# Kernel tuning notes

Hardware: AMD Instinct MI355X
Metric: run time of the kernel (lower is better)

Reference implementation:

```python
import jax, jax.numpy as jnp
import numpy as np

K_KP = 4            # sample_keypoints
RADIUS = 2.0        # sample_radius_m
FEATURE_LEVELS = 2
NUM_HEADS = 8


def _keypoints():
    return jnp.array([[0.0, 0.0, 0.0], [RADIUS, 0.0, 0.0],
                      [0.0, RADIUS, 0.0], [-RADIUS, 0.0, 0.0]], jnp.float32)[:K_KP]


def _bilinear(fmap, grid):
    # fmap [C,H,W], grid [N,2] in [-1,1], align_corners=True, zero padding
    C, H, W = fmap.shape
    x = (grid[:, 0] + 1.0) * 0.5 * (W - 1)
    y = (grid[:, 1] + 1.0) * 0.5 * (H - 1)
    x0 = jnp.floor(x); y0 = jnp.floor(y)
    wx1 = x - x0; wx0 = 1.0 - wx1
    wy1 = y - y0; wy0 = 1.0 - wy1

    def get(xi, yi):
        inb = (xi >= 0) & (xi <= W - 1) & (yi >= 0) & (yi <= H - 1)
        xc = jnp.clip(xi, 0, W - 1).astype(jnp.int32)
        yc = jnp.clip(yi, 0, H - 1).astype(jnp.int32)
        return fmap[:, yc, xc] * inb.astype(fmap.dtype)  # [C,N]

    out = (get(x0, y0) * (wx0 * wy0) + get(x0 + 1, y0) * (wx1 * wy0)
           + get(x0, y0 + 1) * (wx0 * wy1) + get(x0 + 1, y0 + 1) * (wx1 * wy1))
    return out.T  # [N,C]


def _sample_level(fmap, refs, intrinsics, extrinsics):
    # fmap [B,V,C,H,W], refs [B,N,3] with N = Q*K_KP
    B, V, C, H, W = fmap.shape
    N = refs.shape[1]
    ph = jnp.concatenate([refs, jnp.ones((B, N, 1), refs.dtype)], -1)     # [B,N,4]
    cam = jnp.einsum('bvij,bnj->bvni', extrinsics, ph)[..., :3]            # [B,V,N,3]
    uvw = jnp.einsum('bvij,bvnj->bvni', intrinsics, cam)                   # [B,V,N,3]
    z = uvw[..., 2]
    zs = jnp.where(jnp.abs(z) > 1e-6, z, 1e-6)
    gx = 2.0 * (uvw[..., 0] / zs) / (W - 1) - 1.0
    gy = 2.0 * (uvw[..., 1] / zs) / (H - 1) - 1.0
    grid = jnp.stack([gx, gy], -1)                                         # [B,V,N,2]
    samp = jax.vmap(jax.vmap(_bilinear))(fmap, grid)                       # [B,V,N,C]
    valid = (z > 0.0).astype(fmap.dtype)                                   # [B,V,N]
    Q = N // K_KP
    samp = samp.reshape(B, V, Q, K_KP, C)
    valid = valid.reshape(B, V, Q, K_KP)
    s = jnp.einsum('bvqkc,bvqk->bqc', samp, valid)
    cnt = jnp.maximum(valid.sum(axis=(1, 3)), 1.0)[..., None]              # [B,Q,1]
    return s / cnt


def _sampler(features, refs_xyz, intrinsics, extrinsics):
    B, Q = refs_xyz.shape[:2]
    refs = (refs_xyz[:, :, None, :] + _keypoints()[None, None]).reshape(B, Q * K_KP, 3)
    out = jnp.zeros((B, Q, features[0].shape[2]), refs_xyz.dtype)
    for fmap in features[:FEATURE_LEVELS]:
        out = out + _sample_level(fmap, refs, intrinsics, extrinsics)
    return out / float(FEATURE_LEVELS)


def _cross_attn(q_in, ctx, Wq, bq, Wk, bk, Wv, bv, Wo, bo):
    B, Qn, D = q_in.shape
    Kn = ctx.shape[1]
    hd = D // NUM_HEADS
    q = (q_in @ Wq.T + bq).reshape(B, Qn, NUM_HEADS, hd).transpose(0, 2, 1, 3)
    k = (ctx @ Wk.T + bk).reshape(B, Kn, NUM_HEADS, hd).transpose(0, 2, 1, 3)
    v = (ctx @ Wv.T + bv).reshape(B, Kn, NUM_HEADS, hd).transpose(0, 2, 1, 3)
    scores = jnp.einsum('bhqd,bhkd->bhqk', q, k) / jnp.sqrt(jnp.asarray(hd, q.dtype))
    attn = jax.nn.softmax(scores, axis=-1)
    o = jnp.einsum('bhqk,bhkd->bhqd', attn, v).transpose(0, 2, 1, 3).reshape(B, Qn, D)
    return o @ Wo.T + bo


def setup_inputs() -> dict:
    key = jax.random.key(0)
    ks = jax.random.split(key, 10)
    B, V, C, Q = 2, 6, 256, 900
    features0 = jax.random.normal(ks[0], (B, V, C, 64, 176), jnp.float32)
    features1 = jax.random.normal(ks[1], (B, V, C, 32, 88), jnp.float32)
    refs_xyz = jax.random.uniform(ks[2], (B, Q, 3), jnp.float32, -1.0, 1.0) * jnp.array([50.0, 50.0, 1.5])
    K = np.array([[1000.0, 0.0, 800.0], [0.0, 1000.0, 450.0], [0.0, 0.0, 1.0]], np.float32)
    intrinsics = jnp.asarray(np.broadcast_to(K, (B, V, 3, 3)).copy())
    axes = np.array([[0.0, -1.0, 0.0], [0.0, 0.0, -1.0], [1.0, 0.0, 0.0]], np.float32)
    exts = np.zeros((V, 4, 4), np.float32)
    for vi in range(V):
        yaw = 2.0 * np.pi * vi / V
        Rz = np.array([[np.cos(yaw), np.sin(yaw), 0.0], [-np.sin(yaw), np.cos(yaw), 0.0], [0.0, 0.0, 1.0]], np.float32)
        exts[vi, :3, :3] = axes @ Rz
        exts[vi, 3, 3] = 1.0
    extrinsics = jnp.asarray(np.broadcast_to(exts, (B, V, 4, 4)).copy())
    queries = jax.random.normal(ks[3], (B, Q, C), jnp.float32)
    Wq = jax.random.normal(ks[4], (C, C), jnp.float32) * 0.02
    Wk = jax.random.normal(ks[5], (C, C), jnp.float32) * 0.02
    Wv = jax.random.normal(ks[6], (C, C), jnp.float32) * 0.02
    Wo = jax.random.normal(ks[7], (C, C), jnp.float32) * 0.02
    z = jnp.zeros((C,), jnp.float32)
    return {"features0": features0, "features1": features1, "refs_xyz": refs_xyz,
            "intrinsics": intrinsics, "extrinsics": extrinsics, "queries": queries,
            "Wq": Wq, "bq": z, "Wk": Wk, "bk": z, "Wv": Wv, "bv": z, "Wo": Wo, "bo": z}


def reference(features0, features1, refs_xyz, intrinsics, extrinsics, queries,
              Wq, bq, Wk, bk, Wv, bv, Wo, bo):
    sampled = _sampler([features0, features1], refs_xyz, intrinsics, extrinsics)  # [B,Q,C]
    return _cross_attn(queries, sampled, Wq, bq, Wk, bk, Wv, bv, Wo, bo)
```

## Files before the change

kernel.cpp:

```cpp
#include <hip/hip_runtime.h>
#include <math.h>

#define B 2
#define V 6
#define C 256
#define Q 900
#define NH 8
#define HD 32
#define RADIUS 2.0f
#define M_ROWS (B * Q)
#define NT 29
#define SPLITS 4
#define TPS 8

using short8 = __attribute__((ext_vector_type(8))) short;
using f32x4  = __attribute__((ext_vector_type(4))) float;

__device__ __forceinline__ short f2bf(float f) {
    union { float f; unsigned u; } x; x.f = f;
    unsigned r = x.u + 0x7fffu + ((x.u >> 16) & 1u);
    return (short)(r >> 16);
}

__device__ __forceinline__ float kpx(int k) { return (k == 1) ? RADIUS : ((k == 3) ? -RADIUS : 0.f); }
__device__ __forceinline__ float kpy(int k) { return (k == 2) ? RADIUS : 0.f; }

__device__ __forceinline__ float tapv(const float* __restrict__ base, float xi, float yi, int W, int H) {
    if (xi < 0.f || xi > (float)(W - 1) || yi < 0.f || yi > (float)(H - 1)) return 0.f;
    int xc = (int)xi, yc = (int)yi;
    return base[yc * W + xc];
}

__global__ __launch_bounds__(256)
void sampler_kernel(const float* __restrict__ f0, const float* __restrict__ f1,
                    const float* __restrict__ refs, const float* __restrict__ intr,
                    const float* __restrict__ extr, float* __restrict__ sampled)
{
    int b = blockIdx.x / Q, q = blockIdx.x % Q;
    int t = threadIdx.x;
    __shared__ float sx0[2][24], sy0[2][24], swx1[2][24], swy1[2][24];
    __shared__ float sval[24];

    if (t < 48) {
        int lvl = t / 24, pt = t % 24;
        int v = pt >> 2, kp = pt & 3;
        const float* r = refs + (size_t)(b * Q + q) * 3;
        float px = r[0] + kpx(kp), py = r[1] + kpy(kp), pz = r[2];
        const float* E = extr + (size_t)(b * V + v) * 16;
        float cx = E[0] * px + E[1] * py + E[2]  * pz + E[3];
        float cy = E[4] * px + E[5] * py + E[6]  * pz + E[7];
        float cz = E[8] * px + E[9] * py + E[10] * pz + E[11];
        const float* Km = intr + (size_t)(b * V + v) * 9;
        float u = Km[0] * cx + Km[1] * cy + Km[2] * cz;
        float w = Km[3] * cx + Km[4] * cy + Km[5] * cz;
        float z = Km[6] * cx + Km[7] * cy + Km[8] * cz;
        float zs = (fabsf(z) > 1e-6f) ? z : 1e-6f;
        float ru = u / zs, rv = w / zs;
        const float Wf = lvl ? 87.f : 175.f;
        const float Hf = lvl ? 31.f : 63.f;
        float gx = 2.f * ru / Wf - 1.f;
        float gy = 2.f * rv / Hf - 1.f;
        float x = (gx + 1.f) * 0.5f * Wf;
        float y = (gy + 1.f) * 0.5f * Hf;
        float x0 = floorf(x), y0 = floorf(y);
        sx0[lvl][pt] = x0;  sy0[lvl][pt] = y0;
        swx1[lvl][pt] = x - x0;  swy1[lvl][pt] = y - y0;
        if (lvl == 0) sval[pt] = (z > 0.f) ? 1.f : 0.f;
    }
    __syncthreads();

    float cnt = 0.f;
    #pragma unroll
    for (int i = 0; i < 24; ++i) cnt += sval[i];
    cnt = fmaxf(cnt, 1.f);
    float icnt = 1.f / cnt;

    float acc_total = 0.f;
    #pragma unroll
    for (int lvl = 0; lvl < 2; ++lvl) {
        const int H = lvl ? 32 : 64;
        const int W = lvl ? 88 : 176;
        const int HW = H * W;
        const float* fm = lvl ? f1 : f0;

        float accl = 0.f;
        for (int i = 0; i < 24; ++i) {
            if (sval[i] == 0.f) continue;
            int v = i >> 2;
            float x0 = sx0[lvl][i], y0 = sy0[lvl][i];
            float wx1 = swx1[lvl][i], wy1 = swy1[lvl][i];
            float wx0 = 1.f - wx1, wy0 = 1.f - wy1;
            const float* base = fm + ((size_t)(b * V + v) * C + t) * (size_t)HW;
            accl += tapv(base, x0,       y0,       W, H) * (wx0 * wy0)
                  + tapv(base, x0 + 1.f, y0,       W, H) * (wx1 * wy0)
                  + tapv(base, x0,       y0 + 1.f, W, H) * (wx0 * wy1)
                  + tapv(base, x0 + 1.f, y0 + 1.f, W, H) * (wx1 * wy1);
        }
        acc_total += accl * icnt;
    }
    sampled[(size_t)(b * Q + q) * C + t] = acc_total * 0.5f;
}

__global__ __launch_bounds__(256)
void wpack4(const float* __restrict__ W0, const float* __restrict__ W1,
            const float* __restrict__ W2, const float* __restrict__ W3,
            short* __restrict__ P0, short* __restrict__ P1,
            short* __restrict__ P2, short* __restrict__ P3)
{
    int gid = blockIdx.x * 256 + threadIdx.x;
    int mat = gid >> 13;
    int rem = gid & 8191;
    int ks = rem >> 10;
    int nt = (rem >> 6) & 15;
    int lane = rem & 63;
    const float* W = (mat == 0) ? W0 : (mat == 1) ? W1 : (mat == 2) ? W2 : W3;
    short* P = (mat == 0) ? P0 : (mat == 1) ? P1 : (mat == 2) ? P2 : P3;
    int n = nt * 16 + (lane & 15);
    int k0 = ks * 32 + 8 * (lane >> 4);
    float4 a = *(const float4*)(W + (size_t)n * C + k0);
    float4 b = *(const float4*)(W + (size_t)n * C + k0 + 4);
    short8 s;
    s[0] = f2bf(a.x); s[1] = f2bf(a.y); s[2] = f2bf(a.z); s[3] = f2bf(a.w);
    s[4] = f2bf(b.x); s[5] = f2bf(b.y); s[6] = f2bf(b.z); s[7] = f2bf(b.w);
    *(short8*)(P + (size_t)((ks * 16 + nt) * 64 + lane) * 8) = s;
}

__device__ __forceinline__ void mgemm_body(const float* __restrict__ A,
                                           const short* __restrict__ Wp,
                                           const float* __restrict__ bias,
                                           float* __restrict__ Y,
                                           int m0, int n0t)
{
    __shared__ __align__(16) short As[64][264];
    const int tid = threadIdx.x;
    const int lane = tid & 63, w = tid >> 6;
    const int l15 = lane & 15, g = lane >> 4;

    {
        int r = tid & 63, part = tid >> 6;
        int gm = m0 + r;
        #pragma unroll
        for (int c = 0; c < 8; ++c) {
            int k = part * 64 + c * 8;
            float4 x = make_float4(0.f, 0.f, 0.f, 0.f);
            float4 y = make_float4(0.f, 0.f, 0.f, 0.f);
            if (gm < M_ROWS) {
                x = *(const float4*)(A + (size_t)gm * C + k);
                y = *(const float4*)(A + (size_t)gm * C + k + 4);
            }
            short8 s;
            s[0] = f2bf(x.x); s[1] = f2bf(x.y); s[2] = f2bf(x.z); s[3] = f2bf(x.w);
            s[4] = f2bf(y.x); s[5] = f2bf(y.y); s[6] = f2bf(y.z); s[7] = f2bf(y.w);
            *(short8*)&As[r][k] = s;
        }
    }
    __syncthreads();

    f32x4 acc[4];
    #pragma unroll
    for (int c = 0; c < 4; ++c) acc[c] = (f32x4){0.f, 0.f, 0.f, 0.f};

    #pragma unroll
    for (int ks = 0; ks < 8; ++ks) {
        short8 af = *(const short8*)&As[16 * w + l15][ks * 32 + 8 * g];
        #pragma unroll
        for (int c = 0; c < 4; ++c) {
            int nt = n0t * 4 + c;
            short8 bf = *(const short8*)(Wp + (size_t)((ks * 16 + nt) * 64 + lane) * 8);
            acc[c] = __builtin_amdgcn_mfma_f32_16x16x32_bf16(af, bf, acc[c], 0, 0, 0);
        }
    }

    #pragma unroll
    for (int c = 0; c < 4; ++c) {
        int n = n0t * 64 + c * 16 + l15;
        float bv = bias[n];
        #pragma unroll
        for (int j = 0; j < 4; ++j) {
            int gm = m0 + 16 * w + 4 * g + j;
            if (gm < M_ROWS) Y[(size_t)gm * C + n] = acc[c][j] + bv;
        }
    }
}

__global__ __launch_bounds__(256)
void gemm_qkv_mfma(const float* __restrict__ Xq, const float* __restrict__ Xs,
                   const short* __restrict__ Pq, const short* __restrict__ Pk,
                   const short* __restrict__ Pv,
                   const float* __restrict__ bq, const float* __restrict__ bk,
                   const float* __restrict__ bv,
                   float* __restrict__ Yq, float* __restrict__ Yk, float* __restrict__ Yv)
{
    int z = blockIdx.z;
    const float* A    = (z == 0) ? Xq : Xs;
    const short* Wp   = (z == 0) ? Pq : (z == 1) ? Pk : Pv;
    const float* bias = (z == 0) ? bq : (z == 1) ? bk : bv;
    float* Y          = (z == 0) ? Yq : (z == 1) ? Yk : Yv;
    mgemm_body(A, Wp, bias, Y, blockIdx.x * 64, blockIdx.y);
}

__global__ __launch_bounds__(256)
void gemm_o_mfma(const float* __restrict__ A, const short* __restrict__ Wp,
                 const float* __restrict__ bias, float* __restrict__ Y)
{
    mgemm_body(A, Wp, bias, Y, blockIdx.x * 64, blockIdx.y);
}

__global__ __launch_bounds__(128)
void attn_mfma_split(const float* __restrict__ qb, const float* __restrict__ kb,
                     const float* __restrict__ vb,
                     float* __restrict__ Opart, float2* __restrict__ ml)
{
    __shared__ __align__(16) short Ks[2][32][40];
    __shared__ __align__(16) short VT[2][32][36];

    const int tid = threadIdx.x;
    const int lane = tid & 63;
    const int w = tid >> 6;
    const int l15 = lane & 15, g = lane >> 4;
    const int bz = blockIdx.z;
    const int b = bz >> 2, s = bz & 3;
    const int h = blockIdx.y;
    const int q0 = blockIdx.x * 32 + w * 16;
    const int t0 = s * TPS;
    const int t1 = (t0 + TPS < NT) ? (t0 + TPS) : NT;

    short8 qf;
    {
        const float sc = 0.17677669529663687f;
        int qrow = q0 + l15;
        float4 a = make_float4(0.f,0.f,0.f,0.f), c2 = make_float4(0.f,0.f,0.f,0.f);
        if (qrow < Q) {
            const float* p = qb + (size_t)(b * Q + qrow) * C + h * HD + 8 * g;
            a  = *(const float4*)p;
            c2 = *(const float4*)(p + 4);
        }
        qf[0]=f2bf(a.x*sc);  qf[1]=f2bf(a.y*sc);  qf[2]=f2bf(a.z*sc);  qf[3]=f2bf(a.w*sc);
        qf[4]=f2bf(c2.x*sc); qf[5]=f2bf(c2.y*sc); qf[6]=f2bf(c2.z*sc); qf[7]=f2bf(c2.w*sc);
    }

    float m_ = -1e30f, l_ = 0.f;
    f32x4 acc0 = {0.f,0.f,0.f,0.f}, acc1 = {0.f,0.f,0.f,0.f};
    const f32x4 z4 = {0.f,0.f,0.f,0.f};

    const int keyA = tid >> 3,        ccA = tid & 7;
    const int keyB = (128 + tid) >> 3, ccB = tid & 7;
    float4 kregA, vregA, kregB, vregB;

    #define LOAD_TILE(t)                                                        \
    {                                                                           \
        int gkA = (t) * 32 + keyA, gkB = (t) * 32 + keyB;                       \
        if (gkA < Q) {                                                          \
            const float* kp = kb + (size_t)(b*Q+gkA)*C + h*HD + 4*ccA;          \
            const float* vp = vb + (size_t)(b*Q+gkA)*C + h*HD + 4*ccA;          \
            kregA = *(const float4*)kp; vregA = *(const float4*)vp;             \
        } else { kregA = make_float4(0.f,0.f,0.f,0.f); vregA = kregA; }         \
        if (gkB < Q) {                                                          \
            const float* kp = kb + (size_t)(b*Q+gkB)*C + h*HD + 4*ccB;          \
            const float* vp = vb + (size_t)(b*Q+gkB)*C + h*HD + 4*ccB;          \
            kregB = *(const float4*)kp; vregB = *(const float4*)vp;             \
        } else { kregB = make_float4(0.f,0.f,0.f,0.f); vregB = kregB; }         \
    }

    #define WRITE_LDS(bi)                                                       \
    {                                                                           \
        short4 ks;                                                              \
        ks.x = f2bf(kregA.x); ks.y = f2bf(kregA.y); ks.z = f2bf(kregA.z); ks.w = f2bf(kregA.w); \
        *(short4*)&Ks[bi][keyA][4 * ccA] = ks;                                  \
        VT[bi][4*ccA+0][keyA] = f2bf(vregA.x);                                  \
        VT[bi][4*ccA+1][keyA] = f2bf(vregA.y);                                  \
        VT[bi][4*ccA+2][keyA] = f2bf(vregA.z);                                  \
        VT[bi][4*ccA+3][keyA] = f2bf(vregA.w);                                  \
        ks.x = f2bf(kregB.x); ks.y = f2bf(kregB.y); ks.z = f2bf(kregB.z); ks.w = f2bf(kregB.w); \
        *(short4*)&Ks[bi][keyB][4 * ccB] = ks;                                  \
        VT[bi][4*ccB+0][keyB] = f2bf(vregB.x);                                  \
        VT[bi][4*ccB+1][keyB] = f2bf(vregB.y);                                  \
        VT[bi][4*ccB+2][keyB] = f2bf(vregB.z);                                  \
        VT[bi][4*ccB+3][keyB] = f2bf(vregB.w);                                  \
    }

    LOAD_TILE(t0);
    WRITE_LDS(0);
    __syncthreads();

    for (int t = t0; t < t1; ++t) {
        const int buf = (t - t0) & 1;
        if (t + 1 < t1) LOAD_TILE(t + 1);

        short8 kf0 = *(const short8*)&Ks[buf][l15][8 * g];
        short8 kf1 = *(const short8*)&Ks[buf][16 + l15][8 * g];
        f32x4 s0 = __builtin_amdgcn_mfma_f32_16x16x32_bf16(kf0, qf, z4, 0, 0, 0);
        f32x4 s1 = __builtin_amdgcn_mfma_f32_16x16x32_bf16(kf1, qf, z4, 0, 0, 0);

        const int kbase = t * 32;
        if (kbase + 32 > Q) {
            #pragma unroll
            for (int j = 0; j < 4; ++j) {
                if (kbase + 4 * g + j      >= Q) s0[j] = -1e30f;
                if (kbase + 16 + 4 * g + j >= Q) s1[j] = -1e30f;
            }
        }

        float tm = fmaxf(fmaxf(fmaxf(s0[0], s0[1]), fmaxf(s0[2], s0[3])),
                         fmaxf(fmaxf(s1[0], s1[1]), fmaxf(s1[2], s1[3])));
        tm = fmaxf(tm, __shfl_xor(tm, 16));
        tm = fmaxf(tm, __shfl_xor(tm, 32));
        float mn = fmaxf(m_, tm);
        float al = __expf(m_ - mn);
        m_ = mn;
        float p0 = __expf(s0[0]-mn), p1 = __expf(s0[1]-mn), p2 = __expf(s0[2]-mn), p3 = __expf(s0[3]-mn);
        float p4 = __expf(s1[0]-mn), p5 = __expf(s1[1]-mn), p6 = __expf(s1[2]-mn), p7 = __expf(s1[3]-mn);
        float ps = ((p0+p1)+(p2+p3)) + ((p4+p5)+(p6+p7));
        ps += __shfl_xor(ps, 16);
        ps += __shfl_xor(ps, 32);
        l_ = l_ * al + ps;

        #pragma unroll
        for (int j = 0; j < 4; ++j) {
            float alr = __shfl(al, 4 * g + j);
            acc0[j] *= alr;
            acc1[j] *= alr;
        }

        short8 pf;
        pf[0]=f2bf(p0); pf[1]=f2bf(p1); pf[2]=f2bf(p2); pf[3]=f2bf(p3);
        pf[4]=f2bf(p4); pf[5]=f2bf(p5); pf[6]=f2bf(p6); pf[7]=f2bf(p7);

        short4 va  = *(const short4*)&VT[buf][l15][4 * g];
        short4 vb2 = *(const short4*)&VT[buf][l15][16 + 4 * g];
        short4 vc  = *(const short4*)&VT[buf][16 + l15][4 * g];
        short4 vd  = *(const short4*)&VT[buf][16 + l15][16 + 4 * g];
        short8 vf0, vf1;
        vf0[0]=va.x;  vf0[1]=va.y;  vf0[2]=va.z;  vf0[3]=va.w;
        vf0[4]=vb2.x; vf0[5]=vb2.y; vf0[6]=vb2.z; vf0[7]=vb2.w;
        vf1[0]=vc.x;  vf1[1]=vc.y;  vf1[2]=vc.z;  vf1[3]=vc.w;
        vf1[4]=vd.x;  vf1[5]=vd.y;  vf1[6]=vd.z;  vf1[7]=vd.w;
        acc0 = __builtin_amdgcn_mfma_f32_16x16x32_bf16(pf, vf0, acc0, 0, 0, 0);
        acc1 = __builtin_amdgcn_mfma_f32_16x16x32_bf16(pf, vf1, acc1, 0, 0, 0);

        if (t + 1 < t1) WRITE_LDS(buf ^ 1);
        __syncthreads();
    }

    const size_t rowbase = (size_t)((s * B + b) * NH + h) * Q;
    float* op = Opart + rowbase * 32;
    #pragma unroll
    for (int j = 0; j < 4; ++j) {
        int qrow = q0 + 4 * g + j;
        if (qrow < Q) {
            op[(size_t)qrow * 32 + l15]      = acc0[j];
            op[(size_t)qrow * 32 + 16 + l15] = acc1[j];
        }
    }
    if (g == 0 && q0 + l15 < Q) ml[rowbase + q0 + l15] = make_float2(m_, l_);
    #undef LOAD_TILE
    #undef WRITE_LDS
}

__global__ __launch_bounds__(256)
void attn_merge(const float* __restrict__ Opart, const float2* __restrict__ ml,
                float* __restrict__ ob)
{
    const int RBH = B * NH * Q;
    int idx = blockIdx.x * 256 + threadIdx.x;
    int d = idx & 31;
    int r = idx >> 5;
    int b = r / (NH * Q);
    int rem = r - b * (NH * Q);
    int h = rem / Q;
    int q = rem - h * Q;

    float m = -1e30f;
    #pragma unroll
    for (int s = 0; s < SPLITS; ++s) m = fmaxf(m, ml[(size_t)s * RBH + r].x);
    float l = 0.f, o = 0.f;
    #pragma unroll
    for (int s = 0; s < SPLITS; ++s) {
        float2 v = ml[(size_t)s * RBH + r];
        float wgt = __expf(v.x - m);
        l += v.y * wgt;
        o += Opart[((size_t)s * RBH + r) * 32 + d] * wgt;
    }
    ob[((size_t)b * Q + q) * C + h * HD + d] = o / l;
}

extern "C" void kernel_launch(void* const* d_in, const int* in_sizes, int n_in,
                              void* d_out, int out_size, void* d_ws, size_t ws_size,
                              hipStream_t stream) {
    const float* f0   = (const float*)d_in[0];
    const float* f1   = (const float*)d_in[1];
    const float* refs = (const float*)d_in[2];
    const float* intr = (const float*)d_in[3];
    const float* extr = (const float*)d_in[4];
    const float* qin  = (const float*)d_in[5];
    const float* Wq   = (const float*)d_in[6];
    const float* bq   = (const float*)d_in[7];
    const float* Wk   = (const float*)d_in[8];
    const float* bk   = (const float*)d_in[9];
    const float* Wv   = (const float*)d_in[10];
    const float* bv   = (const float*)d_in[11];
    const float* Wo   = (const float*)d_in[12];
    const float* bo   = (const float*)d_in[13];

    float* ws      = (float*)d_ws;
    float* sampled = ws;
    float* qbuf    = sampled + 460800;
    float* kbuf    = qbuf    + 460800;
    float* vbuf    = kbuf    + 460800;
    float* obuf    = vbuf    + 460800;
    short* Pq      = (short*)(obuf + 460800);
    short* Pk      = Pq + 65536;
    short* Pv      = Pk + 65536;
    short* Po      = Pv + 65536;
    float* Opart   = obuf + 460800 + 131072;
    float2* ml     = (float2*)(Opart + (size_t)SPLITS * B * NH * Q * 32);
    float* out     = (float*)d_out;

    wpack4<<<128, 256, 0, stream>>>(Wq, Wk, Wv, Wo, Pq, Pk, Pv, Po);

    sampler_kernel<<<B * Q, 256, 0, stream>>>(f0, f1, refs, intr, extr, sampled);

    dim3 ggrid((M_ROWS + 63) / 64, C / 64, 3);
    gemm_qkv_mfma<<<ggrid, 256, 0, stream>>>(qin, sampled, Pq, Pk, Pv,
                                             bq, bk, bv, qbuf, kbuf, vbuf);

    dim3 agrid((Q + 31) / 32, NH, B * SPLITS);
    attn_mfma_split<<<agrid, 128, 0, stream>>>(qbuf, kbuf, vbuf, Opart, ml);

    attn_merge<<<1800, 256, 0, stream>>>(Opart, ml, obuf);

    dim3 ogrid((M_ROWS + 63) / 64, C / 64, 1);
    gemm_o_mfma<<<ogrid, 256, 0, stream>>>(obuf, Po, bo, out);
}
```

Baseline: 67.63 us.

## Fuse split-attention merge into output GEMM and restructure sampler taps

The separate attn_merge kernel is removed. Its log-sum-exp combine of the split partials now runs in the output projection GEMM prologue, which writes merged rows as bf16 straight into shared memory. This saves one launch and a global round trip of the merged attention output, but every column tile recomputes the merge for its rows. The sampler is also reworked: each thread pair splits the x0/x0+1 taps and handles two channels, then combines results with a lane shuffle. This cuts the bounds checks per thread but makes the gather pattern less coalesced.

Result: faster. 62.79 us (-7.2%).

```diff
diff --git a/kernel.cpp b/kernel.cpp
--- a/kernel.cpp
+++ b/kernel.cpp
@@ -12,6 +12,7 @@
 #define NT 29
 #define SPLITS 4
 #define TPS 8
+#define RBH (B * NH * Q)
 
 using short8 = __attribute__((ext_vector_type(8))) short;
 using f32x4  = __attribute__((ext_vector_type(4))) float;
@@ -24,12 +25,6 @@
 
 __device__ __forceinline__ float kpx(int k) { return (k == 1) ? RADIUS : ((k == 3) ? -RADIUS : 0.f); }
 __device__ __forceinline__ float kpy(int k) { return (k == 2) ? RADIUS : 0.f; }
-
-__device__ __forceinline__ float tapv(const float* __restrict__ base, float xi, float yi, int W, int H) {
-    if (xi < 0.f || xi > (float)(W - 1) || yi < 0.f || yi > (float)(H - 1)) return 0.f;
-    int xc = (int)xi, yc = (int)yi;
-    return base[yc * W + xc];
-}
 
 __global__ __launch_bounds__(256)
 void sampler_kernel(const float* __restrict__ f0, const float* __restrict__ f1,
@@ -75,7 +70,11 @@
     cnt = fmaxf(cnt, 1.f);
     float icnt = 1.f / cnt;
 
-    float acc_total = 0.f;
+    const int xi = t & 1;
+    const int cb = t >> 1;
+    const float xif = (float)xi;
+    float acc0 = 0.f, acc1 = 0.f;
+
     #pragma unroll
     for (int lvl = 0; lvl < 2; ++lvl) {
         const int H = lvl ? 32 : 64;
@@ -83,22 +82,42 @@
         const int HW = H * W;
         const float* fm = lvl ? f1 : f0;
 
-        float accl = 0.f;
+        float a0 = 0.f, a1 = 0.f;
         for (int i = 0; i < 24; ++i) {
             if (sval[i] == 0.f) continue;
             int v = i >> 2;
             float x0 = sx0[lvl][i], y0 = sy0[lvl][i];
-            float wx1 = swx1[lvl][i], wy1 = swy1[lvl][i];
-            float wx0 = 1.f - wx1, wy0 = 1.f - wy1;
-            const float* base = fm + ((size_t)(b * V + v) * C + t) * (size_t)HW;
-            accl += tapv(base, x0,       y0,       W, H) * (wx0 * wy0)
-                  + tapv(base, x0 + 1.f, y0,       W, H) * (wx1 * wy0)
-                  + tapv(base, x0,       y0 + 1.f, W, H) * (wx0 * wy1)
-                  + tapv(base, x0 + 1.f, y0 + 1.f, W, H) * (wx1 * wy1);
-        }
-        acc_total += accl * icnt;
-    }
-    sampled[(size_t)(b * Q + q) * C + t] = acc_total * 0.5f;
+            float wx1v = swx1[lvl][i], wy1v = swy1[lvl][i];
+            float xw = xi ? wx1v : (1.f - wx1v);
+            float wy0v = 1.f - wy1v;
+            float xf = x0 + xif;
+            if (!(xf >= 0.f && xf <= (float)(W - 1))) continue;
+            int xc = (int)xf;
+            const float* bse  = fm + ((size_t)(b * V + v) * C + cb) * (size_t)HW;
+            const float* bse2 = bse + (size_t)128 * HW;
+            if (y0 >= 0.f && y0 <= (float)(H - 1)) {
+                int off = (int)y0 * W + xc;
+                float pw = xw * wy0v;
+                a0 += bse[off]  * pw;
+                a1 += bse2[off] * pw;
+            }
+            float y1 = y0 + 1.f;
+            if (y1 >= 0.f && y1 <= (float)(H - 1)) {
+                int off = (int)y1 * W + xc;
+                float pw = xw * wy1v;
+                a0 += bse[off]  * pw;
+                a1 += bse2[off] * pw;
+            }
+        }
+        acc0 += a0 * icnt;
+        acc1 += a1 * icnt;
+    }
+    acc0 *= 0.5f; acc1 *= 0.5f;
+    acc0 += __shfl_xor(acc0, 1);
+    acc1 += __shfl_xor(acc1, 1);
+    float* outp = sampled + (size_t)(b * Q + q) * C;
+    if (xi == 0) outp[cb] = acc0;
+    else         outp[cb + 128] = acc1;
 }
 
 __global__ __launch_bounds__(256)
@@ -200,10 +219,95 @@
 }
 
 __global__ __launch_bounds__(256)
-void gemm_o_mfma(const float* __restrict__ A, const short* __restrict__ Wp,
-                 const float* __restrict__ bias, float* __restrict__ Y)
+void gemm_o_merge(const float* __restrict__ Opart, const float2* __restrict__ ml,
+                  const short* __restrict__ Wp, const float* __restrict__ bias,
+                  float* __restrict__ Y)
 {
-    mgemm_body(A, Wp, bias, Y, blockIdx.x * 64, blockIdx.y);
+    __shared__ __align__(16) short As[64][264];
+    const int tid = threadIdx.x;
+    const int lane = tid & 63, w = tid >> 6;
+    const int l15 = lane & 15, g = lane >> 4;
+    const int m0 = blockIdx.x * 64, n0t = blockIdx.y;
+
+    {
+        int r = tid & 63, part = tid >> 6;
+        int gm = m0 + r;
+        if (gm < M_ROWS) {
+            int bb = (gm >= Q) ? 1 : 0;
+            int qq = gm - bb * Q;
+            #pragma unroll
+            for (int hh = 0; hh < 2; ++hh) {
+                int h = 2 * part + hh;
+                int rrow = (bb * NH + h) * Q + qq;
+                float2 v[SPLITS];
+                float m = -1e30f;
+                #pragma unroll
+                for (int s = 0; s < SPLITS; ++s) {
+                    v[s] = ml[(size_t)s * RBH + rrow];
+                    m = fmaxf(m, v[s].x);
+                }
+                float l = 0.f, wgt[SPLITS];
+                #pragma unroll
+                for (int s = 0; s < SPLITS; ++s) {
+                    wgt[s] = __expf(v[s].x - m);
+                    l += v[s].y * wgt[s];
+                }
+                float invl = 1.f / l;
+                #pragma unroll
+                for (int cc = 0; cc < 4; ++cc) {
+                    int d0 = cc * 8;
+                    float o[8] = {0.f,0.f,0.f,0.f,0.f,0.f,0.f,0.f};
+                    #pragma unroll
+                    for (int s = 0; s < SPLITS; ++s) {
+                        const float* op = Opart + ((size_t)s * RBH + rrow) * 32 + d0;
+                        float4 x = *(const float4*)op;
+                        float4 y = *(const float4*)(op + 4);
+                        o[0] += x.x * wgt[s]; o[1] += x.y * wgt[s];
+                        o[2] += x.z * wgt[s]; o[3] += x.w * wgt[s];
+                        o[4] += y.x * wgt[s]; o[5] += y.y * wgt[s];
+                        o[6] += y.z * wgt[s]; o[7] += y.w * wgt[s];
+                    }
+                    short8 sv;
+                    #pragma unroll
+                    for (int j = 0; j < 8; ++j) sv[j] = f2bf(o[j] * invl);
+                    *(short8*)&As[r][part * 64 + hh * 32 + d0] = sv;
+                }
+            }
+        } else {
+            #pragma unroll
+            for (int c = 0; c < 8; ++c) {
+                short8 z = {0,0,0,0,0,0,0,0};
+                *(short8*)&As[r][part * 64 + c * 8] = z;
+            }
+        }
+    }
+    __syncthreads();
+
+    f32x4 acc[4];
+    #pragma unroll
+    for (int c = 0; c < 4; ++c) acc[c] = (f32x4){0.f, 0.f, 0.f, 0.f};
+
+    #pragma unroll
+    for (int ks = 0; ks < 8; ++ks) {
+        short8 af = *(const short8*)&As[16 * w + l15][ks * 32 + 8 * g];
+        #pragma unroll
+        for (int c = 0; c < 4; ++c) {
+            int nt = n0t * 4 + c;
+            short8 bf = *(const short8*)(Wp + (size_t)((ks * 16 + nt) * 64 + lane) * 8);
+            acc[c] = __builtin_amdgcn_mfma_f32_16x16x32_bf16(af, bf, acc[c], 0, 0, 0);
+        }
+    }
+
+    #pragma unroll
+    for (int c = 0; c < 4; ++c) {
+        int n = n0t * 64 + c * 16 + l15;
+        float bv = bias[n];
+        #pragma unroll
+        for (int j = 0; j < 4; ++j) {
+            int gm = m0 + 16 * w + 4 * g + j;
+            if (gm < M_ROWS) Y[(size_t)gm * C + n] = acc[c][j] + bv;
+        }
+    }
 }
 
 __global__ __launch_bounds__(128)
@@ -355,33 +459,6 @@
     if (g == 0 && q0 + l15 < Q) ml[rowbase + q0 + l15] = make_float2(m_, l_);
     #undef LOAD_TILE
     #undef WRITE_LDS
-}
-
-__global__ __launch_bounds__(256)
-void attn_merge(const float* __restrict__ Opart, const float2* __restrict__ ml,
-                float* __restrict__ ob)
-{
-    const int RBH = B * NH * Q;
-    int idx = blockIdx.x * 256 + threadIdx.x;
-    int d = idx & 31;
-    int r = idx >> 5;
-    int b = r / (NH * Q);
-    int rem = r - b * (NH * Q);
-    int h = rem / Q;
-    int q = rem - h * Q;
-
-    float m = -1e30f;
-    #pragma unroll
-    for (int s = 0; s < SPLITS; ++s) m = fmaxf(m, ml[(size_t)s * RBH + r].x);
-    float l = 0.f, o = 0.f;
-    #pragma unroll
-    for (int s = 0; s < SPLITS; ++s) {
-        float2 v = ml[(size_t)s * RBH + r];
-        float wgt = __expf(v.x - m);
-        l += v.y * wgt;
-        o += Opart[((size_t)s * RBH + r) * 32 + d] * wgt;
-    }
-    ob[((size_t)b * Q + q) * C + h * HD + d] = o / l;
 }
 
 extern "C" void kernel_launch(void* const* d_in, const int* in_sizes, int n_in,
@@ -413,7 +490,7 @@
     short* Pv      = Pk + 65536;
     short* Po      = Pv + 65536;
     float* Opart   = obuf + 460800 + 131072;
-    float2* ml     = (float2*)(Opart + (size_t)SPLITS * B * NH * Q * 32);
+    float2* ml     = (float2*)(Opart + (size_t)SPLITS * RBH * 32);
     float* out     = (float*)d_out;
 
     wpack4<<<128, 256, 0, stream>>>(Wq, Wk, Wv, Wo, Pq, Pk, Pv, Po);
@@ -427,8 +504,6 @@
     dim3 agrid((Q + 31) / 32, NH, B * SPLITS);
     attn_mfma_split<<<agrid, 128, 0, stream>>>(qbuf, kbuf, vbuf, Opart, ml);
 
-    attn_merge<<<1800, 256, 0, stream>>>(Opart, ml, obuf);
-
     dim3 ogrid((M_ROWS + 63) / 64, C / 64, 1);
-    gemm_o_mfma<<<ogrid, 256, 0, stream>>>(obuf, Po, bo, out);
-}
+    gemm_o_merge<<<ogrid, 256, 0, stream>>>(Opart, ml, Po, bo, out);
+}
```
